# Kernel tuning notes

Measured on AMD Instinct MI355X. Metric: run time of the kernel, lower is better.

Reference implementation:

```python
import jax, jax.numpy as jnp
import numpy as np

N_HEAD = 16
D_HEAD = 64
N_GROUPS = 4
D_EMBED = 1024
ROPE_N = 32
B, T = 2, 2048


def apply_rope(x, cos, sin):
    # x: (..., T, ROPE_N); cos/sin: (T, ROPE_N) broadcast over leading dims
    h = x.shape[-1]
    x1, x2 = x[..., : h // 2], x[..., h // 2 :]
    rotated = jnp.concatenate((-x2, x1), axis=-1)
    return (x * cos + rotated * sin).astype(x.dtype)


def setup_inputs() -> dict:
    key = jax.random.key(0)
    k1, k2, k3, k4, k5 = jax.random.split(key, 5)
    return {
        "x": jax.random.normal(k1, (B, T, D_EMBED), dtype=jnp.float32),
        "cos": jax.random.uniform(k2, (T, ROPE_N), dtype=jnp.float32),
        "sin": jax.random.uniform(k3, (T, ROPE_N), dtype=jnp.float32),
        "mask": jnp.ones((B, T), dtype=bool),  # unused by the original forward (passes None to SDPA)
        "Wqkv": jax.random.normal(k4, (D_EMBED, (N_HEAD + 2 * N_GROUPS) * D_HEAD), dtype=jnp.float32) * 0.02,
        "Wout": jax.random.normal(k5, (N_HEAD * D_HEAD, D_EMBED), dtype=jnp.float32) * 0.02,
    }


def reference(x, cos, sin, mask, Wqkv, Wout):
    Bv, Tv, _ = x.shape
    q_per_kv = N_HEAD // N_GROUPS  # 4
    total_qkv = q_per_kv + 2       # 6

    qkv = jnp.einsum("btc,cf->btf", x, Wqkv)  # (B, T, 1536)
    qkv = qkv.reshape(Bv, Tv, N_GROUPS, total_qkv, D_HEAD)
    qkv = jnp.transpose(qkv, (0, 2, 3, 1, 4))  # (B, G, total_qkv, T, d)

    q = qkv[:, :, :q_per_kv]           # (B, G, q_per_kv, T, d)
    k = qkv[:, :, q_per_kv : q_per_kv + 1]  # (B, G, 1, T, d)
    v = qkv[:, :, q_per_kv + 1 :]           # (B, G, 1, T, d)

    # GQA expand (1 < groups < heads)
    k = jnp.broadcast_to(k, (Bv, N_GROUPS, q_per_kv, Tv, D_HEAD))
    v = jnp.broadcast_to(v, (Bv, N_GROUPS, q_per_kv, Tv, D_HEAD))

    q = q.reshape(Bv, N_HEAD, Tv, D_HEAD)
    k = k.reshape(Bv, N_HEAD, Tv, D_HEAD)
    v = v.reshape(Bv, N_HEAD, Tv, D_HEAD)

    # partial RoPE on the first ROPE_N dims of each head
    q = jnp.concatenate((apply_rope(q[..., :ROPE_N], cos, sin), q[..., ROPE_N:]), axis=-1)
    k = jnp.concatenate((apply_rope(k[..., :ROPE_N], cos, sin), k[..., ROPE_N:]), axis=-1)

    scale = 1.0 / np.sqrt(D_HEAD).astype(np.float32)
    scores = jnp.einsum("bhtd,bhsd->bhts", q, k) * scale
    attn = jax.nn.softmax(scores, axis=-1)
    y = jnp.einsum("bhts,bhsd->bhtd", attn, v)   # (B, H, T, d)
    y = jnp.transpose(y, (0, 2, 1, 3)).reshape(Bv, Tv, N_HEAD * D_HEAD)
    return jnp.einsum("btf,fc->btc", y, Wout)
```

## Files before the change

kernel.cpp:

```cpp
#include <hip/hip_runtime.h>
#include <hip/hip_bf16.h>
#include <math.h>

#define BATCH   2
#define TSEQ    2048
#define DEMBED  1024
#define NHEAD   16
#define DHEAD   64
#define NGROUP  4
#define ROPEN   32
#define FQKV    1536
#define MROWS   (BATCH*TSEQ)

typedef __attribute__((ext_vector_type(8))) short short8;
typedef __attribute__((ext_vector_type(4))) float floatx4;

__device__ __forceinline__ void split_pack8(const float* f, uint4& h4, uint4& l4) {
    uint u[8], lu[8];
    #pragma unroll
    for (int j = 0; j < 8; ++j) {
        u[j] = __float_as_uint(f[j]);
        float lf = f[j] - __uint_as_float(u[j] & 0xffff0000u);
        lu[j] = __float_as_uint(lf);
    }
    h4.x = __builtin_amdgcn_perm(u[1], u[0], 0x07060302u);
    h4.y = __builtin_amdgcn_perm(u[3], u[2], 0x07060302u);
    h4.z = __builtin_amdgcn_perm(u[5], u[4], 0x07060302u);
    h4.w = __builtin_amdgcn_perm(u[7], u[6], 0x07060302u);
    l4.x = __builtin_amdgcn_perm(lu[1], lu[0], 0x07060302u);
    l4.y = __builtin_amdgcn_perm(lu[3], lu[2], 0x07060302u);
    l4.z = __builtin_amdgcn_perm(lu[5], lu[4], 0x07060302u);
    l4.w = __builtin_amdgcn_perm(lu[7], lu[6], 0x07060302u);
}

__device__ __forceinline__ void rtn_pack8(const float* f, uint4& h4) {
    uint t[8];
    #pragma unroll
    for (int j = 0; j < 8; ++j)
        t[j] = __float_as_uint(f[j]) + 0x8000u;
    h4.x = __builtin_amdgcn_perm(t[1], t[0], 0x07060302u);
    h4.y = __builtin_amdgcn_perm(t[3], t[2], 0x07060302u);
    h4.z = __builtin_amdgcn_perm(t[5], t[4], 0x07060302u);
    h4.w = __builtin_amdgcn_perm(t[7], t[6], 0x07060302u);
}

__device__ __forceinline__ uint pk_bf16x2(float f0, float f1) {
    uint u0 = __float_as_uint(f0) + 0x8000u;
    uint u1 = __float_as_uint(f1) + 0x8000u;
    return __builtin_amdgcn_perm(u1, u0, 0x07060302u);
}

__device__ __forceinline__ float fast_exp2(float x) {
    float r;
    asm("v_exp_f32 %0, %1" : "=v"(r) : "v"(x));
    return r;
}

__device__ __forceinline__ void lds_async16(void* lds, const void* gp) {
    __builtin_amdgcn_global_load_lds(
        (const __attribute__((address_space(1))) unsigned int*)gp,
        (__attribute__((address_space(3))) unsigned int*)lds,
        16, 0, 0);
}


__device__ __forceinline__ void conv_xy_body(const float* __restrict__ in,
                                             char* __restrict__ img,
                                             int bid, int tid) {
    const int c   = bid & 15;
    const int mt  = bid >> 4;
    const int r    = tid >> 1;
    const int half = tid & 1;

    const float* src = in + (size_t)(mt*128 + r)*1024 + c*64 + half*32;
    float f[32];
    #pragma unroll
    for (int u = 0; u < 8; ++u)
        *(float4*)(f + 4*u) = *(const float4*)(src + 4*u);

    char* tile = img + ((size_t)(mt*16 + c)) * 32768;
    #pragma unroll
    for (int cc = 0; cc < 4; ++cc) {
        uint4 h4, l4;
        split_pack8(f + cc*8, h4, l4);
        int j    = half*4 + cc;
        int phys = j ^ (r & 7);
        *(uint4*)(tile + r*128 + phys*16)         = h4;
        *(uint4*)(tile + 16384 + r*128 + phys*16) = l4;
    }
}

__device__ __forceinline__ void conv_w_body(const float* __restrict__ W,
                                            int N, char* __restrict__ img,
                                            int c, int nt, int tid,
                                            float (*Lf)[132]) {
    {
        const int kk = tid >> 2;
        const int nc = (tid & 3) * 32;
        const float* src = W + (size_t)(c*64 + kk)*N + nt*128 + nc;
        #pragma unroll
        for (int u = 0; u < 8; ++u)
            *(float4*)(&Lf[kk][nc + 4*u]) = *(const float4*)(src + 4*u);
    }
    __syncthreads();

    char* tile = img + ((size_t)(nt*16 + c)) * 32768;
    #pragma unroll
    for (int rep = 0; rep < 4; ++rep) {
        int idx = rep*256 + tid;
        int n = idx & 127;
        int j = idx >> 7;
        float v[8];
        #pragma unroll
        for (int i = 0; i < 8; ++i) v[i] = Lf[j*8 + i][n];
        uint4 h4, l4;
        split_pack8(v, h4, l4);
        int phys = j ^ (n & 7);
        *(uint4*)(tile + n*128 + phys*16)         = h4;
        *(uint4*)(tile + 16384 + n*128 + phys*16) = l4;
    }
}

__global__ __launch_bounds__(256) void conv_all(const float* __restrict__ x,
                                                const float* __restrict__ Wqkv,
                                                const float* __restrict__ Wout,
                                                char* __restrict__ Ximg,
                                                char* __restrict__ Bq,
                                                char* __restrict__ Bo) {
    __shared__ float Lf[64][132];
    const int bid = blockIdx.x;
    const int tid = threadIdx.x;
    if (bid < 512) {
        conv_xy_body(x, Ximg, bid, tid);
    } else if (bid < 704) {
        const int idx = bid - 512;
        conv_w_body(Wqkv, FQKV, Bq, idx & 15, idx >> 4, tid, Lf);
    } else {
        const int idx = bid - 704;
        conv_w_body(Wout, DEMBED, Bo, idx & 15, idx >> 4, tid, Lf);
    }
}

struct GemmAcc { floatx4 a[4][4]; };

__device__ __forceinline__ void gemm_mfma_core(const char* __restrict__ Aimg,
                                               const char* __restrict__ Bimg,
                                               char* smem, int mt, int nt,
                                               int tid, GemmAcc& G) {
    const int wv = tid >> 6;
    const int wm = wv & 1, wn = wv >> 1;
    const int lane = tid & 63;
    const int qd = lane >> 4, cl = lane & 15;
    const int wslot = (tid & 192) * 16;

    #pragma unroll
    for (int tm = 0; tm < 4; ++tm)
        #pragma unroll
        for (int tn = 0; tn < 4; ++tn)
            G.a[tm][tn] = (floatx4){0.f, 0.f, 0.f, 0.f};

    for (int c = 0; c < 16; ++c) {
        __syncthreads();
        {
            const uint4* gA = (const uint4*)(Aimg + ((size_t)(mt*16 + c)) * 32768) + tid;
            const uint4* gB = (const uint4*)(Bimg + ((size_t)(nt*16 + c)) * 32768) + tid;
            #pragma unroll
            for (int j = 0; j < 8; ++j) {
                lds_async16(smem + j*4096 + wslot,         gA + j*256);
                lds_async16(smem + 32768 + j*4096 + wslot, gB + j*256);
            }
        }
        __syncthreads();

        #pragma unroll
        for (int s = 0; s < 2; ++s) {
            const int phys = ((s*4 + qd) ^ (cl & 7)) * 16;
            short8 ah[4], al[4], bh[4], bl[4];
            #pragma unroll
            for (int tt = 0; tt < 4; ++tt) {
                const int rA = wm*64 + 16*tt + cl;
                ah[tt] = *(const short8*)(smem + rA*128 + phys);
                al[tt] = *(const short8*)(smem + 16384 + rA*128 + phys);
                const int rB = wn*64 + 16*tt + cl;
                bh[tt] = *(const short8*)(smem + 32768 + rB*128 + phys);
                bl[tt] = *(const short8*)(smem + 49152 + rB*128 + phys);
            }
            #pragma unroll
            for (int tm = 0; tm < 4; ++tm)
                #pragma unroll
                for (int tn = 0; tn < 4; ++tn) {
                    G.a[tm][tn] = __builtin_amdgcn_mfma_f32_16x16x32_bf16(ah[tm], bh[tn], G.a[tm][tn], 0, 0, 0);
                    G.a[tm][tn] = __builtin_amdgcn_mfma_f32_16x16x32_bf16(al[tm], bh[tn], G.a[tm][tn], 0, 0, 0);
                    G.a[tm][tn] = __builtin_amdgcn_mfma_f32_16x16x32_bf16(ah[tm], bl[tn], G.a[tm][tn], 0, 0, 0);
                }
        }
    }
}

__global__ __launch_bounds__(256, 2) void gemm_qkv_mfma(const char* __restrict__ Aimg,
                                                        const char* __restrict__ Bimg,
                                                        const float* __restrict__ cosp,
                                                        const float* __restrict__ sinp,
                                                        float* __restrict__ Qf,
                                                        ushort* __restrict__ Kimg,
                                                        ushort* __restrict__ Vimg) {
    __shared__ __align__(16) char smem[68608];
    const int tid = threadIdx.x;
    const int nt = blockIdx.x, mt = blockIdx.y;

    GemmAcc G;
    gemm_mfma_core(Aimg, Bimg, smem, mt, nt, tid, G);

    const int wv = tid >> 6;
    const int wm = wv & 1, wn = wv >> 1;
    const int lane = tid & 63;
    const int qd = lane >> 4, cl = lane & 15;

    const int slice = nt*2 + wn;
    const int g  = slice / 6;
    const int jj = slice % 6;
    const int b  = mt >> 4;

    if (jj != 5) {
        #pragma unroll
        for (int tm = 0; tm < 4; ++tm)
            #pragma unroll
            for (int r = 0; r < 4; ++r) {
                int m = mt*128 + wm*64 + 16*tm + 4*qd + r;
                int t = m & 2047;
                float c1 = cosp[t*ROPEN + cl],      s1 = sinp[t*ROPEN + cl];
                float c2 = cosp[t*ROPEN + 16 + cl], s2 = sinp[t*ROPEN + 16 + cl];
                float x1 = G.a[tm][0][r], x2 = G.a[tm][1][r];
                G.a[tm][0][r] = x1*c1 - x2*s1;
                G.a[tm][1][r] = x2*c2 + x1*s2;
            }
    }

    if (jj < 4) {
        #pragma unroll
        for (int tm = 0; tm < 4; ++tm)
            #pragma unroll
            for (int tn = 0; tn < 4; ++tn)
                #pragma unroll
                for (int r = 0; r < 4; ++r) {
                    int m = mt*128 + wm*64 + 16*tm + 4*qd + r;
                    Qf[(size_t)m*1024 + (g*4 + jj)*64 + 16*tn + cl] = G.a[tm][tn][r];
                }
    } else {
        float* Lw = (float*)(smem + wv*17152);
        __syncthreads();
        #pragma unroll
        for (int tm = 0; tm < 4; ++tm)
            #pragma unroll
            for (int tn = 0; tn < 4; ++tn)
                #pragma unroll
                for (int r = 0; r < 4; ++r)
                    Lw[(16*tm + 4*qd + r)*67 + 16*tn + cl] = G.a[tm][tn][r];
        __syncthreads();

        const int cloc = (mt & 15)*2 + wm;
        ushort* img = ((jj == 4) ? Kimg : Vimg)
                      + (size_t)(b*4 + g)*262144 + (size_t)cloc*8192;
        if (jj == 4) {
            const int rr = lane;
            float f[8];
            #pragma unroll
            for (int ch = 0; ch < 8; ++ch) {
                *(float4*)f       = *(const float4*)(&Lw[rr*67 + ch*8]);
                *(float4*)(f + 4) = *(const float4*)(&Lw[rr*67 + ch*8 + 4]);
                uint4 h4, l4;
                split_pack8(f, h4, l4);
                int phys = ch ^ (rr & 7);
                *(uint4*)(img + rr*64 + phys*8)        = h4;
                *(uint4*)(img + 4096 + rr*64 + phys*8) = l4;
            }
        } else {
            const int d = lane;
            float f[8];
            #pragma unroll
            for (int ch = 0; ch < 8; ++ch) {
                const int kb = 32*(ch >> 2) + 4*(ch & 3);
                #pragma unroll
                for (int i = 0; i < 4; ++i) f[i]     = Lw[(kb + i)*67 + d];
                #pragma unroll
                for (int i = 0; i < 4; ++i) f[4 + i] = Lw[(kb + 16 + i)*67 + d];
                uint4 h4;
                rtn_pack8(f, h4);
                int phys = ch ^ (d & 7);
                *(uint4*)(img + d*64 + phys*8) = h4;
            }
        }
    }
}

__global__ __launch_bounds__(256, 2) void gemm_out_mfma(const char* __restrict__ Aimg,
                                                        const char* __restrict__ Bimg,
                                                        float* __restrict__ C) {
    __shared__ __align__(16) char smem[49152];
    const int tid = threadIdx.x;
    const int nt = blockIdx.x, mt = blockIdx.y;

    const int wv = tid >> 6;
    const int wm = wv & 1, wn = wv >> 1;
    const int lane = tid & 63;
    const int qd = lane >> 4, cl = lane & 15;
    const int wslot = (tid & 192) * 16;

    floatx4 acc[2][4];
    #pragma unroll
    for (int tm = 0; tm < 2; ++tm)
        #pragma unroll
        for (int tn = 0; tn < 4; ++tn)
            acc[tm][tn] = (floatx4){0.f, 0.f, 0.f, 0.f};

    for (int c = 0; c < 16; ++c) {
        __syncthreads();
        {
            const char* sA = Aimg + ((size_t)((mt >> 1)*16 + c))*32768
                                  + (mt & 1)*8192 + (size_t)tid*16;
            const char* sB = Bimg + ((size_t)(nt*16 + c))*32768 + (size_t)tid*16;
            lds_async16(smem + wslot,          sA);
            lds_async16(smem + 4096  + wslot,  sA + 4096);
            lds_async16(smem + 8192  + wslot,  sA + 16384);
            lds_async16(smem + 12288 + wslot,  sA + 16384 + 4096);
            #pragma unroll
            for (int j = 0; j < 4; ++j) {
                lds_async16(smem + 16384 + j*4096 + wslot, sB + j*4096);
                lds_async16(smem + 32768 + j*4096 + wslot, sB + 16384 + j*4096);
            }
        }
        __syncthreads();

        #pragma unroll
        for (int s = 0; s < 2; ++s) {
            const int phys = ((s*4 + qd) ^ (cl & 7)) * 16;
            short8 ah[2], al[2], bh[4], bl[4];
            #pragma unroll
            for (int tt = 0; tt < 2; ++tt) {
                const int rA = wm*32 + 16*tt + cl;
                ah[tt] = *(const short8*)(smem + rA*128 + phys);
                al[tt] = *(const short8*)(smem + 8192 + rA*128 + phys);
            }
            #pragma unroll
            for (int tt = 0; tt < 4; ++tt) {
                const int rB = wn*64 + 16*tt + cl;
                bh[tt] = *(const short8*)(smem + 16384 + rB*128 + phys);
                bl[tt] = *(const short8*)(smem + 32768 + rB*128 + phys);
            }
            #pragma unroll
            for (int tm = 0; tm < 2; ++tm)
                #pragma unroll
                for (int tn = 0; tn < 4; ++tn) {
                    acc[tm][tn] = __builtin_amdgcn_mfma_f32_16x16x32_bf16(ah[tm], bh[tn], acc[tm][tn], 0, 0, 0);
                    acc[tm][tn] = __builtin_amdgcn_mfma_f32_16x16x32_bf16(al[tm], bh[tn], acc[tm][tn], 0, 0, 0);
                    acc[tm][tn] = __builtin_amdgcn_mfma_f32_16x16x32_bf16(ah[tm], bl[tn], acc[tm][tn], 0, 0, 0);
                }
        }
    }

    #pragma unroll
    for (int tm = 0; tm < 2; ++tm)
        #pragma unroll
        for (int tn = 0; tn < 4; ++tn)
            #pragma unroll
            for (int r = 0; r < 4; ++r) {
                int m = mt*64 + wm*32 + 16*tm + 4*qd + r;
                int n = nt*128 + wn*64 + 16*tn + cl;
                C[(size_t)m*1024 + n] = acc[tm][tn][r];
            }
}

__global__ __launch_bounds__(512, 4) void attn15(const float* __restrict__ Qf,
                                                 const char* __restrict__ Kimg,
                                                 const char* __restrict__ Vimg,
                                                 char* __restrict__ Yimg) {
    __shared__ __align__(16) char smem[49152];

    const int tid  = threadIdx.x;
    const int wv8  = tid >> 6;
    const int grp  = wv8 >> 2;
    const int wq   = wv8 & 3;
    const int lane = tid & 63;
    const int qd   = lane >> 4;
    const int cl   = lane & 15;

    const int bg    = blockIdx.x & 7;
    const int inner = blockIdx.x >> 3;
    const int hj    = inner >> 4;
    const int qt    = inner & 15;
    const int b = bg >> 2, g = bg & 3;
    const int h = g*4 + hj;

    short8 qh[2][2], ql[2][2];
    #pragma unroll
    for (int rb = 0; rb < 2; ++rb) {
        const float* qp = Qf + (size_t)(b*2048 + qt*128 + wq*32 + rb*16 + cl)*1024
                             + h*64 + 8*qd;
        #pragma unroll
        for (int s = 0; s < 2; ++s) {
            float f[8];
            *(float4*)f       = *(const float4*)(qp + 32*s);
            *(float4*)(f + 4) = *(const float4*)(qp + 32*s + 4);
            #pragma unroll
            for (int i = 0; i < 8; ++i) f[i] *= 0.125f * 1.44269504088896f;
            uint4 h4, l4;
            split_pack8(f, h4, l4);
            qh[rb][s] = __builtin_bit_cast(short8, h4);
            ql[rb][s] = __builtin_bit_cast(short8, l4);
        }
    }

    floatx4 accOT[2][4] = {};
    float lsum[2] = {};

    const char* Kg0 = Kimg + (size_t)bg*524288;
    const char* Vg0 = Vimg + (size_t)bg*524288;
    const int wslot = wv8 << 10;

    int voff[4];
    #pragma unroll
    for (int tt = 0; tt < 4; ++tt)
        voff[tt] = (16*tt + cl)*128 + (((4*grp + qd) ^ (cl & 7))*16);

    {
        const char* ksrc = Kg0 + (size_t)tid*16;
        lds_async16(smem + wslot,        ksrc);
        lds_async16(smem + 8192 + wslot, ksrc + 8192);
        lds_async16(smem + 32768 + wslot, Vg0 + (size_t)tid*16);
    }

    for (int c = 0; c < TSEQ/64; ++c) {
        __syncthreads();
        const int buf = c & 1;

        if (c + 1 < TSEQ/64) {
            const char* ksrc = Kg0 + (size_t)(c+1)*16384 + (size_t)tid*16;
            const char* vsrc = Vg0 + (size_t)(c+1)*16384 + (size_t)tid*16;
            lds_async16(smem + (1-buf)*16384 + wslot,        ksrc);
            lds_async16(smem + (1-buf)*16384 + 8192 + wslot, ksrc + 8192);
            lds_async16(smem + 32768 + (1-buf)*8192 + wslot, vsrc);
        }
        const char* Kl = smem + buf*16384;
        const char* Vl = smem + 32768 + buf*8192;

        floatx4 accST[2][2] = {};
        __builtin_amdgcn_s_setprio(1);
        #pragma unroll
        for (int s = 0; s < 2; ++s) {
            #pragma unroll
            for (int tt = 0; tt < 2; ++tt) {
                const int off = (32*grp + 16*tt + cl)*128
                              + (((4*s + qd) ^ (cl & 7))*16);
                short8 kh = *(const short8*)(Kl + off);
                short8 kl = *(const short8*)(Kl + 8192 + off);
                #pragma unroll
                for (int rb = 0; rb < 2; ++rb) {
                    accST[rb][tt] = __builtin_amdgcn_mfma_f32_16x16x32_bf16(kh, qh[rb][s], accST[rb][tt], 0, 0, 0);
                    accST[rb][tt] = __builtin_amdgcn_mfma_f32_16x16x32_bf16(kh, ql[rb][s], accST[rb][tt], 0, 0, 0);
                    accST[rb][tt] = __builtin_amdgcn_mfma_f32_16x16x32_bf16(kl, qh[rb][s], accST[rb][tt], 0, 0, 0);
                }
            }
        }
        __builtin_amdgcn_s_setprio(0);

        short8 pa[2];
        #pragma unroll
        for (int rb = 0; rb < 2; ++rb) {
            float p[8];
            #pragma unroll
            for (int tt = 0; tt < 2; ++tt)
                #pragma unroll
                for (int r = 0; r < 4; ++r)
                    p[4*tt + r] = fast_exp2(accST[rb][tt][r]);
            lsum[rb] += ((p[0] + p[1]) + (p[2] + p[3]))
                      + ((p[4] + p[5]) + (p[6] + p[7]));
            uint4 paw;
            paw.x = pk_bf16x2(p[0], p[1]);
            paw.y = pk_bf16x2(p[2], p[3]);
            paw.z = pk_bf16x2(p[4], p[5]);
            paw.w = pk_bf16x2(p[6], p[7]);
            pa[rb] = __builtin_bit_cast(short8, paw);
        }

        __builtin_amdgcn_s_setprio(1);
        #pragma unroll
        for (int tt = 0; tt < 4; ++tt) {
            short8 vh = *(const short8*)(Vl + voff[tt]);
            #pragma unroll
            for (int rb = 0; rb < 2; ++rb)
                accOT[rb][tt] = __builtin_amdgcn_mfma_f32_16x16x32_bf16(vh, pa[rb], accOT[rb][tt], 0, 0, 0);
        }
        __builtin_amdgcn_s_setprio(0);
    }

    __syncthreads();
    float* Pb = (float*)smem;
    if (grp == 1) {
        #pragma unroll
        for (int rb = 0; rb < 2; ++rb) {
            float* dst = Pb + (size_t)(((wq*2 + rb)*64) + lane)*17;
            #pragma unroll
            for (int tt = 0; tt < 4; ++tt)
                #pragma unroll
                for (int r = 0; r < 4; ++r)
                    dst[4*tt + r] = accOT[rb][tt][r];
            dst[16] = lsum[rb];
        }
    }
    __syncthreads();
    float inv[2] = {1.f, 1.f};
    if (grp == 0) {
        #pragma unroll
        for (int rb = 0; rb < 2; ++rb) {
            const float* sp = Pb + (size_t)(((wq*2 + rb)*64) + lane)*17;
            #pragma unroll
            for (int tt = 0; tt < 4; ++tt)
                #pragma unroll
                for (int r = 0; r < 4; ++r)
                    accOT[rb][tt][r] += sp[4*tt + r];
            float l = lsum[rb] + sp[16];
            l += __shfl_xor(l, 16);
            l += __shfl_xor(l, 32);
            inv[rb] = 1.0f / l;
        }
    }
    __syncthreads();
    float* Lt = (float*)smem;
    if (grp == 0) {
        #pragma unroll
        for (int rb = 0; rb < 2; ++rb) {
            const int row = wq*32 + rb*16 + cl;
            #pragma unroll
            for (int tt = 0; tt < 4; ++tt)
                #pragma unroll
                for (int r = 0; r < 4; ++r)
                    Lt[row*66 + 16*tt + 4*qd + r] = accOT[rb][tt][r] * inv[rb];
        }
    }
    __syncthreads();
    {
        char* tile = Yimg + (size_t)((b*16 + qt)*16 + h) * 32768;
        #pragma unroll
        for (int cc = 0; cc < 2; ++cc) {
            const int idx = tid*2 + cc;
            const int r0 = idx >> 3;
            const int j  = idx & 7;
            float f[8];
            #pragma unroll
            for (int u = 0; u < 4; ++u)
                *(float2*)(f + 2*u) = *(const float2*)(&Lt[r0*66 + j*8 + 2*u]);
            uint4 h4, l4;
            split_pack8(f, h4, l4);
            int phys = j ^ (r0 & 7);
            *(uint4*)(tile + r0*128 + phys*16)         = h4;
            *(uint4*)(tile + 16384 + r0*128 + phys*16) = l4;
        }
    }
}

extern "C" void kernel_launch(void* const* d_in, const int* in_sizes, int n_in,
                              void* d_out, int out_size, void* d_ws, size_t ws_size,
                              hipStream_t stream) {
    const float* x    = (const float*)d_in[0];
    const float* cosp = (const float*)d_in[1];
    const float* sinp = (const float*)d_in[2];
    const float* Wqkv = (const float*)d_in[4];
    const float* Wout = (const float*)d_in[5];
    float* out = (float*)d_out;

    char* ws = (char*)d_ws;
    float*  Qf    = (float*)(ws);
    ushort* Kimg  = (ushort*)(ws + ((size_t)16<<20));
    ushort* Vimg  = (ushort*)(ws + ((size_t)20<<20));
    char*   Bo    = ws + ((size_t)24<<20);
    char*   Ximg  = ws + ((size_t)28<<20);
    char*   Bq    = ws + ((size_t)44<<20);
    char*   Yimg  = ws + ((size_t)28<<20);

    conv_all<<<832, 256, 0, stream>>>(x, Wqkv, Wout, Ximg, Bq, Bo);
    gemm_qkv_mfma<<<dim3(12, 32), 256, 0, stream>>>(Ximg, Bq, cosp, sinp,
                                                    Qf, Kimg, Vimg);
    attn15<<<512, 512, 0, stream>>>(Qf, (const char*)Kimg, (const char*)Vimg,
                                    Yimg);
    gemm_out_mfma<<<dim3(8, 64), 256, 0, stream>>>(Yimg, Bo, out);
}
```

Measured before the change: 221.3 us.

## Double-buffer GEMM K-chunks with 32-wide split-bf16 tile images

Reorganizes the packed hi/lo bf16 operand images from 64-wide K chunks into 32-wide chunks with a new XOR swizzle. Both MFMA GEMMs now double-buffer shared memory, prefetching the next chunk asynchronously while computing on the current one. This drops one barrier per iteration and aims to overlap global-to-LDS loads with MFMA work. In exchange there are twice as many loop iterations, and the producers (conversion kernel and attention epilogue) must write the new layout consistently.

```diff
diff --git a/kernel.cpp b/kernel.cpp
--- a/kernel.cpp
+++ b/kernel.cpp
@@ -78,15 +78,15 @@
     for (int u = 0; u < 8; ++u)
         *(float4*)(f + 4*u) = *(const float4*)(src + 4*u);
 
-    char* tile = img + ((size_t)(mt*16 + c)) * 32768;
+    char* reg = img + (size_t)(mt*32 + c*2 + half) * 16384;
+    const int pr = (r >> 1) & 3;
     #pragma unroll
     for (int cc = 0; cc < 4; ++cc) {
         uint4 h4, l4;
         split_pack8(f + cc*8, h4, l4);
-        int j    = half*4 + cc;
-        int phys = j ^ (r & 7);
-        *(uint4*)(tile + r*128 + phys*16)         = h4;
-        *(uint4*)(tile + 16384 + r*128 + phys*16) = l4;
+        int slot = cc ^ pr;
+        *(uint4*)(reg + r*64 + slot*16)        = h4;
+        *(uint4*)(reg + 8192 + r*64 + slot*16) = l4;
     }
 }
 
@@ -104,7 +104,7 @@
     }
     __syncthreads();
 
-    char* tile = img + ((size_t)(nt*16 + c)) * 32768;
+    char* tbase = img + (size_t)(nt*32 + c*2) * 16384;
     #pragma unroll
     for (int rep = 0; rep < 4; ++rep) {
         int idx = rep*256 + tid;
@@ -115,9 +115,10 @@
         for (int i = 0; i < 8; ++i) v[i] = Lf[j*8 + i][n];
         uint4 h4, l4;
         split_pack8(v, h4, l4);
-        int phys = j ^ (n & 7);
-        *(uint4*)(tile + n*128 + phys*16)         = h4;
-        *(uint4*)(tile + 16384 + n*128 + phys*16) = l4;
+        char* reg = tbase + (j >> 2)*16384;
+        int slot = (j & 3) ^ ((n >> 1) & 3);
+        *(uint4*)(reg + n*64 + slot*16)        = h4;
+        *(uint4*)(reg + 8192 + n*64 + slot*16) = l4;
     }
 }
 
@@ -152,6 +153,7 @@
     const int lane = tid & 63;
     const int qd = lane >> 4, cl = lane & 15;
     const int wslot = (tid & 192) * 16;
+    const int slotx = (cl >> 1) & 3;
 
     #pragma unroll
     for (int tm = 0; tm < 4; ++tm)
@@ -159,41 +161,49 @@
         for (int tn = 0; tn < 4; ++tn)
             G.a[tm][tn] = (floatx4){0.f, 0.f, 0.f, 0.f};
 
-    for (int c = 0; c < 16; ++c) {
+    {
+        const char* srcA = Aimg + (size_t)(mt*32) * 16384 + (size_t)tid*16;
+        const char* srcB = Bimg + (size_t)(nt*32) * 16384 + (size_t)tid*16;
+        #pragma unroll
+        for (int j = 0; j < 4; ++j) {
+            lds_async16(smem + j*4096 + wslot,         srcA + j*4096);
+            lds_async16(smem + 16384 + j*4096 + wslot, srcB + j*4096);
+        }
+    }
+
+    for (int c = 0; c < 32; ++c) {
         __syncthreads();
-        {
-            const uint4* gA = (const uint4*)(Aimg + ((size_t)(mt*16 + c)) * 32768) + tid;
-            const uint4* gB = (const uint4*)(Bimg + ((size_t)(nt*16 + c)) * 32768) + tid;
-            #pragma unroll
-            for (int j = 0; j < 8; ++j) {
-                lds_async16(smem + j*4096 + wslot,         gA + j*256);
-                lds_async16(smem + 32768 + j*4096 + wslot, gB + j*256);
-            }
-        }
-        __syncthreads();
-
-        #pragma unroll
-        for (int s = 0; s < 2; ++s) {
-            const int phys = ((s*4 + qd) ^ (cl & 7)) * 16;
-            short8 ah[4], al[4], bh[4], bl[4];
-            #pragma unroll
-            for (int tt = 0; tt < 4; ++tt) {
-                const int rA = wm*64 + 16*tt + cl;
-                ah[tt] = *(const short8*)(smem + rA*128 + phys);
-                al[tt] = *(const short8*)(smem + 16384 + rA*128 + phys);
-                const int rB = wn*64 + 16*tt + cl;
-                bh[tt] = *(const short8*)(smem + 32768 + rB*128 + phys);
-                bl[tt] = *(const short8*)(smem + 49152 + rB*128 + phys);
-            }
-            #pragma unroll
-            for (int tm = 0; tm < 4; ++tm)
-                #pragma unroll
-                for (int tn = 0; tn < 4; ++tn) {
-                    G.a[tm][tn] = __builtin_amdgcn_mfma_f32_16x16x32_bf16(ah[tm], bh[tn], G.a[tm][tn], 0, 0, 0);
-                    G.a[tm][tn] = __builtin_amdgcn_mfma_f32_16x16x32_bf16(al[tm], bh[tn], G.a[tm][tn], 0, 0, 0);
-                    G.a[tm][tn] = __builtin_amdgcn_mfma_f32_16x16x32_bf16(ah[tm], bl[tn], G.a[tm][tn], 0, 0, 0);
-                }
-        }
+        const int buf = c & 1;
+        if (c + 1 < 32) {
+            const char* srcA = Aimg + (size_t)(mt*32 + c+1)*16384 + (size_t)tid*16;
+            const char* srcB = Bimg + (size_t)(nt*32 + c+1)*16384 + (size_t)tid*16;
+            char* dst = smem + (1 - buf)*32768;
+            #pragma unroll
+            for (int j = 0; j < 4; ++j) {
+                lds_async16(dst + j*4096 + wslot,         srcA + j*4096);
+                lds_async16(dst + 16384 + j*4096 + wslot, srcB + j*4096);
+            }
+        }
+        const char* S = smem + buf*32768;
+
+        short8 ah[4], al[4], bh[4], bl[4];
+        #pragma unroll
+        for (int tt = 0; tt < 4; ++tt) {
+            const int ra = (wm*64 + 16*tt + cl)*64 + ((qd ^ slotx)*16);
+            ah[tt] = *(const short8*)(S + ra);
+            al[tt] = *(const short8*)(S + 8192 + ra);
+            const int rb = (wn*64 + 16*tt + cl)*64 + ((qd ^ slotx)*16);
+            bh[tt] = *(const short8*)(S + 16384 + rb);
+            bl[tt] = *(const short8*)(S + 24576 + rb);
+        }
+        #pragma unroll
+        for (int tm = 0; tm < 4; ++tm)
+            #pragma unroll
+            for (int tn = 0; tn < 4; ++tn) {
+                G.a[tm][tn] = __builtin_amdgcn_mfma_f32_16x16x32_bf16(ah[tm], bh[tn], G.a[tm][tn], 0, 0, 0);
+                G.a[tm][tn] = __builtin_amdgcn_mfma_f32_16x16x32_bf16(al[tm], bh[tn], G.a[tm][tn], 0, 0, 0);
+                G.a[tm][tn] = __builtin_amdgcn_mfma_f32_16x16x32_bf16(ah[tm], bl[tn], G.a[tm][tn], 0, 0, 0);
+            }
     }
 }
 
@@ -305,6 +315,8 @@
     const int lane = tid & 63;
     const int qd = lane >> 4, cl = lane & 15;
     const int wslot = (tid & 192) * 16;
+    const int slotx = (cl >> 1) & 3;
+    const int ahalf = (mt & 1) * 4096;
 
     floatx4 acc[2][4];
     #pragma unroll
@@ -313,49 +325,52 @@
         for (int tn = 0; tn < 4; ++tn)
             acc[tm][tn] = (floatx4){0.f, 0.f, 0.f, 0.f};
 
-    for (int c = 0; c < 16; ++c) {
+    {
+        const char* gA = Aimg + (size_t)((mt >> 1)*32)*16384 + (size_t)tid*16;
+        const char* gB = Bimg + (size_t)(nt*32)*16384 + (size_t)tid*16;
+        lds_async16(smem + wslot,        gA + ahalf);
+        lds_async16(smem + 4096 + wslot, gA + 8192 + ahalf);
+        #pragma unroll
+        for (int j = 0; j < 4; ++j)
+            lds_async16(smem + 8192 + j*4096 + wslot, gB + j*4096);
+    }
+
+    for (int c = 0; c < 32; ++c) {
         __syncthreads();
-        {
-            const char* sA = Aimg + ((size_t)((mt >> 1)*16 + c))*32768
-                                  + (mt & 1)*8192 + (size_t)tid*16;
-            const char* sB = Bimg + ((size_t)(nt*16 + c))*32768 + (size_t)tid*16;
-            lds_async16(smem + wslot,          sA);
-            lds_async16(smem + 4096  + wslot,  sA + 4096);
-            lds_async16(smem + 8192  + wslot,  sA + 16384);
-            lds_async16(smem + 12288 + wslot,  sA + 16384 + 4096);
-            #pragma unroll
-            for (int j = 0; j < 4; ++j) {
-                lds_async16(smem + 16384 + j*4096 + wslot, sB + j*4096);
-                lds_async16(smem + 32768 + j*4096 + wslot, sB + 16384 + j*4096);
-            }
-        }
-        __syncthreads();
-
-        #pragma unroll
-        for (int s = 0; s < 2; ++s) {
-            const int phys = ((s*4 + qd) ^ (cl & 7)) * 16;
-            short8 ah[2], al[2], bh[4], bl[4];
-            #pragma unroll
-            for (int tt = 0; tt < 2; ++tt) {
-                const int rA = wm*32 + 16*tt + cl;
-                ah[tt] = *(const short8*)(smem + rA*128 + phys);
-                al[tt] = *(const short8*)(smem + 8192 + rA*128 + phys);
-            }
-            #pragma unroll
-            for (int tt = 0; tt < 4; ++tt) {
-                const int rB = wn*64 + 16*tt + cl;
-                bh[tt] = *(const short8*)(smem + 16384 + rB*128 + phys);
-                bl[tt] = *(const short8*)(smem + 32768 + rB*128 + phys);
-            }
-            #pragma unroll
-            for (int tm = 0; tm < 2; ++tm)
-                #pragma unroll
-                for (int tn = 0; tn < 4; ++tn) {
-                    acc[tm][tn] = __builtin_amdgcn_mfma_f32_16x16x32_bf16(ah[tm], bh[tn], acc[tm][tn], 0, 0, 0);
-                    acc[tm][tn] = __builtin_amdgcn_mfma_f32_16x16x32_bf16(al[tm], bh[tn], acc[tm][tn], 0, 0, 0);
-                    acc[tm][tn] = __builtin_amdgcn_mfma_f32_16x16x32_bf16(ah[tm], bl[tn], acc[tm][tn], 0, 0, 0);
-                }
-        }
+        const int buf = c & 1;
+        if (c + 1 < 32) {
+            const char* gA = Aimg + (size_t)((mt >> 1)*32 + c+1)*16384 + (size_t)tid*16;
+            const char* gB = Bimg + (size_t)(nt*32 + c+1)*16384 + (size_t)tid*16;
+            char* dst = smem + (1 - buf)*24576;
+            lds_async16(dst + wslot,        gA + ahalf);
+            lds_async16(dst + 4096 + wslot, gA + 8192 + ahalf);
+            #pragma unroll
+            for (int j = 0; j < 4; ++j)
+                lds_async16(dst + 8192 + j*4096 + wslot, gB + j*4096);
+        }
+        const char* S = smem + buf*24576;
+
+        short8 ah[2], al[2], bh[4], bl[4];
+        #pragma unroll
+        for (int tt = 0; tt < 2; ++tt) {
+            const int ra = (wm*32 + 16*tt + cl)*64 + ((qd ^ slotx)*16);
+            ah[tt] = *(const short8*)(S + ra);
+            al[tt] = *(const short8*)(S + 4096 + ra);
+        }
+        #pragma unroll
+        for (int tt = 0; tt < 4; ++tt) {
+            const int rb = (wn*64 + 16*tt + cl)*64 + ((qd ^ slotx)*16);
+            bh[tt] = *(const short8*)(S + 8192 + rb);
+            bl[tt] = *(const short8*)(S + 16384 + rb);
+        }
+        #pragma unroll
+        for (int tm = 0; tm < 2; ++tm)
+            #pragma unroll
+            for (int tn = 0; tn < 4; ++tn) {
+                acc[tm][tn] = __builtin_amdgcn_mfma_f32_16x16x32_bf16(ah[tm], bh[tn], acc[tm][tn], 0, 0, 0);
+                acc[tm][tn] = __builtin_amdgcn_mfma_f32_16x16x32_bf16(al[tm], bh[tn], acc[tm][tn], 0, 0, 0);
+                acc[tm][tn] = __builtin_amdgcn_mfma_f32_16x16x32_bf16(ah[tm], bl[tn], acc[tm][tn], 0, 0, 0);
+            }
     }
 
     #pragma unroll
@@ -539,7 +554,7 @@
     }
     __syncthreads();
     {
-        char* tile = Yimg + (size_t)((b*16 + qt)*16 + h) * 32768;
+        char* tbase = Yimg + ((size_t)(b*16 + qt)*32 + 2*h) * 16384;
         #pragma unroll
         for (int cc = 0; cc < 2; ++cc) {
             const int idx = tid*2 + cc;
@@ -551,9 +566,10 @@
                 *(float2*)(f + 2*u) = *(const float2*)(&Lt[r0*66 + j*8 + 2*u]);
             uint4 h4, l4;
             split_pack8(f, h4, l4);
-            int phys = j ^ (r0 & 7);
-            *(uint4*)(tile + r0*128 + phys*16)         = h4;
-            *(uint4*)(tile + 16384 + r0*128 + phys*16) = l4;
+            char* reg = tbase + (j >> 2)*16384;
+            int slot = (j & 3) ^ ((r0 >> 1) & 3);
+            *(uint4*)(reg + r0*64 + slot*16)        = h4;
+            *(uint4*)(reg + 8192 + r0*64 + slot*16) = l4;
         }
     }
 }
```

New measurement: 212.9 us. 3.8% less time.
